# Performance work log

Hardware: AMD Instinct MI355X
Metric: run time of the kernel (lower is better)

## Reference

```python
import jax, jax.numpy as jnp
import numpy as np

V = 45      # vocab / input_size / output_size
H = 2048    # hidden_size
W = 128     # stack_width
D = 200     # stack_depth


def setup_inputs() -> dict:
    key = jax.random.key(0)
    ks = jax.random.split(key, 14)
    s = 0.02
    return {
        "inp": jax.random.randint(ks[0], (1,), 0, V),
        "hidden": jax.random.normal(ks[1], (1, 1, H), jnp.float32),
        "stack": jax.random.normal(ks[2], (1, D, W), jnp.float32),
        "emb": jax.random.normal(ks[3], (V, H), jnp.float32) * s,
        "ctrl_W": jax.random.normal(ks[4], (3, H), jnp.float32) * s,
        "ctrl_b": jnp.zeros((3,), jnp.float32),
        "sin_W": jax.random.normal(ks[5], (W, H), jnp.float32) * s,
        "sin_b": jnp.zeros((W,), jnp.float32),
        "w_ih": jax.random.normal(ks[6], (3 * H, H + W), jnp.float32) * s,
        "w_hh": jax.random.normal(ks[7], (3 * H, H), jnp.float32) * s,
        "b_ih": jnp.zeros((3 * H,), jnp.float32),
        "b_hh": jnp.zeros((3 * H,), jnp.float32),
        "dec_W": jax.random.normal(ks[8], (V, H), jnp.float32) * s,
        "dec_b": jnp.zeros((V,), jnp.float32),
    }


def reference(inp, hidden, stack, emb, ctrl_W, ctrl_b, sin_W, sin_b,
              w_ih, w_hh, b_ih, b_hh, dec_W, dec_b):
    h = hidden[0]  # [1, H]  (n_layers=1, unidirectional -> squeeze(0))

    # --- differentiable stack update ---
    controls = jax.nn.softmax(h @ ctrl_W.T + ctrl_b, axis=1)      # [1, 3]
    stack_input = jnp.tanh(h @ sin_W.T + sin_b)[:, None, :]       # [1, 1, W]
    zeros_bottom = jnp.zeros((1, 1, W), stack.dtype)
    stack_down = jnp.concatenate([stack[:, 1:], zeros_bottom], axis=1)   # pop
    stack_up = jnp.concatenate([stack_input, stack[:, :-1]], axis=1)    # push
    c = controls.reshape(1, 3, 1, 1)  # (push, pop, no_op)
    new_stack = c[:, 2] * stack + c[:, 0] * stack_up + c[:, 1] * stack_down
    stack_top = new_stack[:, 0, :]  # [1, W]

    # --- embed token, concat stack top ---
    x = jnp.concatenate([emb[inp].reshape(1, -1), stack_top], axis=1)  # [1, H+W]

    # --- GRU cell (PyTorch gate convention) ---
    gi = x @ w_ih.T + b_ih   # [1, 3H]
    gh = h @ w_hh.T + b_hh   # [1, 3H]
    i_r, i_z, i_n = jnp.split(gi, 3, axis=1)
    h_r, h_z, h_n = jnp.split(gh, 3, axis=1)
    r = jax.nn.sigmoid(i_r + h_r)
    z = jax.nn.sigmoid(i_z + h_z)
    n = jnp.tanh(i_n + r * h_n)
    h_new = (1.0 - z) * n + z * h   # [1, H]

    # --- decoder ---
    output = h_new @ dec_W.T + dec_b  # [1, V]
    return output, h_new[None], new_stack
```

## Files before the change

kernel.cpp:

```cpp
#include <hip/hip_runtime.h>

#define V_SZ 45
#define H_SZ 2048
#define W_SZ 128
#define D_SZ 200
#define X_SZ (H_SZ + W_SZ)
#define STACK_BLKS ((D_SZ * W_SZ) / 256)

#define WS_CTRL 0
#define WS_SIN  16
#define WS_HNEW 160

typedef float f4 __attribute__((ext_vector_type(4)));

__device__ __forceinline__ float dot4(f4 a, f4 b) {
  return a.x * b.x + a.y * b.y + a.z * b.z + a.w * b.w;
}

__device__ __forceinline__ f4 ldnt(const f4* p) {
  return __builtin_nontemporal_load(p);
}

__device__ __forceinline__ float wave_reduce(float v) {
#pragma unroll
  for (int o = 32; o > 0; o >>= 1) v += __shfl_down(v, o, 64);
  return v;
}

__device__ __forceinline__ void ctrl_softmax(const float* __restrict__ ws,
                                             float& c0, float& c1, float& c2) {
  const float l0 = ws[WS_CTRL + 0], l1 = ws[WS_CTRL + 1], l2 = ws[WS_CTRL + 2];
  const float m = fmaxf(l0, fmaxf(l1, l2));
  const float e0 = __expf(l0 - m), e1 = __expf(l1 - m), e2 = __expf(l2 - m);
  const float inv = 1.f / (e0 + e1 + e2);
  c0 = e0 * inv; c1 = e1 * inv; c2 = e2 * inv;
}

__global__ __launch_bounds__(256) void k1_small_gemv(
    const float* __restrict__ hidden,
    const float* __restrict__ ctrl_W,
    const float* __restrict__ ctrl_b,
    const float* __restrict__ sin_W,
    const float* __restrict__ sin_b,
    float* __restrict__ ws) {
  const int b = blockIdx.x;
  const int tid = threadIdx.x;
  const float* row = (b < 3) ? (ctrl_W + (size_t)b * H_SZ)
                             : (sin_W + (size_t)(b - 3) * H_SZ);
  const f4* rw4 = (const f4*)row;
  const f4* rh4 = (const f4*)hidden;
  float acc = dot4(rw4[tid], rh4[tid]) + dot4(rw4[tid + 256], rh4[tid + 256]);

  acc = wave_reduce(acc);
  __shared__ float red[4];
  const int wv_id = tid >> 6;
  if ((tid & 63) == 0) red[wv_id] = acc;
  __syncthreads();
  if (tid == 0) {
    float total = red[0] + red[1] + red[2] + red[3];
    if (b < 3) {
      ws[WS_CTRL + b] = total + ctrl_b[b];
    } else {
      ws[WS_SIN + (b - 3)] = tanhf(total + sin_b[b - 3]);
    }
  }
}

__global__ __launch_bounds__(256) void k3_gru_stack(
    const int* __restrict__ inp,
    const float* __restrict__ hidden,
    const float* __restrict__ emb,
    const float* __restrict__ stack,
    const float* __restrict__ w_ih,
    const float* __restrict__ w_hh,
    const float* __restrict__ b_ih,
    const float* __restrict__ b_hh,
    float* __restrict__ ws,
    float* __restrict__ out) {
  const int tid = threadIdx.x;

  if (blockIdx.x < STACK_BLKS) {
    const int i = blockIdx.x * 256 + tid;
    float c0, c1, c2;
    ctrl_softmax(ws, c0, c1, c2);
    const int d = i >> 7;
    const int w = i & (W_SZ - 1);
    const float s = stack[i];
    const float up = (d == 0) ? ws[WS_SIN + w] : stack[i - W_SZ];
    const float dn = (d == D_SZ - 1) ? 0.f : stack[i + W_SZ];
    out[V_SZ + H_SZ + i] = c2 * s + c0 * up + c1 * dn;
    return;
  }

  const int j = blockIdx.x - STACK_BLKS;

  float bi0 = 0.f, bi1 = 0.f, bi2 = 0.f;
  float bh0 = 0.f, bh1 = 0.f, bh2 = 0.f, hj = 0.f;
  if (tid == 0) {
    bi0 = b_ih[j]; bi1 = b_ih[j + H_SZ]; bi2 = b_ih[j + 2 * H_SZ];
    bh0 = b_hh[j]; bh1 = b_hh[j + H_SZ]; bh2 = b_hh[j + 2 * H_SZ];
    hj  = hidden[j];
  }

  float a0 = 0.f, a1 = 0.f, a2 = 0.f, a3 = 0.f, a4 = 0.f, a5 = 0.f;

  const f4* wi0 = (const f4*)(w_ih + (size_t)j * X_SZ);
  const f4* wi1 = (const f4*)(w_ih + (size_t)(j + H_SZ) * X_SZ);
  const f4* wi2 = (const f4*)(w_ih + (size_t)(j + 2 * H_SZ) * X_SZ);
  const f4* emb4 = (const f4*)(emb + (size_t)inp[0] * H_SZ);

#pragma unroll
  for (int q = 0; q < 2; ++q) {
    const int c = tid + q * 256;
    const f4 xv = emb4[c];
    a0 += dot4(ldnt(wi0 + c), xv);
    a1 += dot4(ldnt(wi1 + c), xv);
    a2 += dot4(ldnt(wi2 + c), xv);
  }
  if (tid < (X_SZ - H_SZ) / 4) {
    const int c = 512 + tid;
    const int w = 4 * tid;
    float c0, c1, c2;
    ctrl_softmax(ws, c0, c1, c2);
    const f4 s0 = *(const f4*)(stack + w);
    const f4 s1 = *(const f4*)(stack + W_SZ + w);
    const f4 sv = *(const f4*)(ws + WS_SIN + w);
    f4 xv;
    xv.x = c2 * s0.x + c0 * sv.x + c1 * s1.x;
    xv.y = c2 * s0.y + c0 * sv.y + c1 * s1.y;
    xv.z = c2 * s0.z + c0 * sv.z + c1 * s1.z;
    xv.w = c2 * s0.w + c0 * sv.w + c1 * s1.w;
    a0 += dot4(ldnt(wi0 + c), xv);
    a1 += dot4(ldnt(wi1 + c), xv);
    a2 += dot4(ldnt(wi2 + c), xv);
  }

  const f4* wh0 = (const f4*)(w_hh + (size_t)j * H_SZ);
  const f4* wh1 = (const f4*)(w_hh + (size_t)(j + H_SZ) * H_SZ);
  const f4* wh2 = (const f4*)(w_hh + (size_t)(j + 2 * H_SZ) * H_SZ);
  const f4* h4 = (const f4*)hidden;
#pragma unroll
  for (int q = 0; q < 2; ++q) {
    const int c = tid + q * 256;
    const f4 hv = h4[c];
    a3 += dot4(ldnt(wh0 + c), hv);
    a4 += dot4(ldnt(wh1 + c), hv);
    a5 += dot4(ldnt(wh2 + c), hv);
  }

  a0 = wave_reduce(a0); a1 = wave_reduce(a1); a2 = wave_reduce(a2);
  a3 = wave_reduce(a3); a4 = wave_reduce(a4); a5 = wave_reduce(a5);
  __shared__ float red[4][6];
  const int wv_id = tid >> 6;
  if ((tid & 63) == 0) {
    red[wv_id][0] = a0; red[wv_id][1] = a1; red[wv_id][2] = a2;
    red[wv_id][3] = a3; red[wv_id][4] = a4; red[wv_id][5] = a5;
  }
  __syncthreads();
  if (tid == 0) {
    float t[6];
#pragma unroll
    for (int q = 0; q < 6; ++q)
      t[q] = red[0][q] + red[1][q] + red[2][q] + red[3][q];
    const float gi_r = t[0] + bi0;
    const float gi_z = t[1] + bi1;
    const float gi_n = t[2] + bi2;
    const float gh_r = t[3] + bh0;
    const float gh_z = t[4] + bh1;
    const float gh_n = t[5] + bh2;
    const float r = 1.f / (1.f + __expf(-(gi_r + gh_r)));
    const float z = 1.f / (1.f + __expf(-(gi_z + gh_z)));
    const float n = tanhf(gi_n + r * gh_n);
    const float hn = (1.f - z) * n + z * hj;
    ws[WS_HNEW + j] = hn;
    out[V_SZ + j] = hn;
  }
}

__global__ __launch_bounds__(256) void k4_dec(
    const float* __restrict__ dec_W,
    const float* __restrict__ dec_b,
    const float* __restrict__ ws,
    float* __restrict__ out) {
  const int v = blockIdx.x;
  const int tid = threadIdx.x;
  float db = 0.f;
  if (tid == 0) db = dec_b[v];
  const f4* row = (const f4*)(dec_W + (size_t)v * H_SZ);
  const f4* h4 = (const f4*)(ws + WS_HNEW);
  float acc = dot4(row[tid], h4[tid]) + dot4(row[tid + 256], h4[tid + 256]);
  acc = wave_reduce(acc);
  __shared__ float red[4];
  const int wv_id = tid >> 6;
  if ((tid & 63) == 0) red[wv_id] = acc;
  __syncthreads();
  if (tid == 0) out[v] = red[0] + red[1] + red[2] + red[3] + db;
}

extern "C" void kernel_launch(void* const* d_in, const int* in_sizes, int n_in,
                              void* d_out, int out_size, void* d_ws, size_t ws_size,
                              hipStream_t stream) {
  const int*   inp    = (const int*)d_in[0];
  const float* hidden = (const float*)d_in[1];
  const float* stack  = (const float*)d_in[2];
  const float* emb    = (const float*)d_in[3];
  const float* ctrl_W = (const float*)d_in[4];
  const float* ctrl_b = (const float*)d_in[5];
  const float* sin_W  = (const float*)d_in[6];
  const float* sin_b  = (const float*)d_in[7];
  const float* w_ih   = (const float*)d_in[8];
  const float* w_hh   = (const float*)d_in[9];
  const float* b_ih   = (const float*)d_in[10];
  const float* b_hh   = (const float*)d_in[11];
  const float* dec_W  = (const float*)d_in[12];
  const float* dec_b  = (const float*)d_in[13];
  float* out = (float*)d_out;
  float* ws = (float*)d_ws;

  k1_small_gemv<<<3 + W_SZ, 256, 0, stream>>>(hidden, ctrl_W, ctrl_b, sin_W, sin_b, ws);
  k3_gru_stack<<<STACK_BLKS + H_SZ, 256, 0, stream>>>(inp, hidden, emb, stack,
                                                      w_ih, w_hh, b_ih, b_hh, ws, out);
  k4_dec<<<V_SZ, 256, 0, stream>>>(dec_W, dec_b, ws, out);
}
```

Before: 156.2 us.

## Overlap control GEMV with hidden/embedding GRU partial sums, finish stack part later

Moves the large GRU GEMV work that does not depend on the stack (embedding part of w_ih and all of w_hh) into the first kernel, which now runs alongside the control/stack-input GEMV. Partial gate sums go to workspace. A second kernel does the stack update, the 128-wide stack-top slice of w_ih (one wave per hidden unit) and the gate nonlinearities. This removes the serial dependency of the big weight stream on the small first kernel. In exchange it adds a workspace round trip for 6 partials per unit and a separate pass over the w_ih tail columns.

```diff
diff --git a/kernel.cpp b/kernel.cpp
--- a/kernel.cpp
+++ b/kernel.cpp
@@ -6,10 +6,13 @@
 #define D_SZ 200
 #define X_SZ (H_SZ + W_SZ)
 #define STACK_BLKS ((D_SZ * W_SZ) / 256)
+#define K1_BLKS (3 + W_SZ)
+#define GATE_JPB 4
+#define GATE_BLKS (H_SZ / GATE_JPB)
 
 #define WS_CTRL 0
 #define WS_SIN  16
-#define WS_HNEW 160
+#define WS_PART 160
 
 typedef float f4 __attribute__((ext_vector_type(4)));
 
@@ -24,6 +27,12 @@
 __device__ __forceinline__ float wave_reduce(float v) {
 #pragma unroll
   for (int o = 32; o > 0; o >>= 1) v += __shfl_down(v, o, 64);
+  return v;
+}
+
+__device__ __forceinline__ float half_reduce(float v) {
+#pragma unroll
+  for (int o = 16; o > 0; o >>= 1) v += __shfl_down(v, o, 32);
   return v;
 }
 
@@ -36,45 +45,101 @@
   c0 = e0 * inv; c1 = e1 * inv; c2 = e2 * inv;
 }
 
-__global__ __launch_bounds__(256) void k1_small_gemv(
+__global__ __launch_bounds__(256) void kA(
+    const int* __restrict__ inp,
     const float* __restrict__ hidden,
+    const float* __restrict__ emb,
     const float* __restrict__ ctrl_W,
     const float* __restrict__ ctrl_b,
     const float* __restrict__ sin_W,
     const float* __restrict__ sin_b,
-    float* __restrict__ ws) {
-  const int b = blockIdx.x;
-  const int tid = threadIdx.x;
-  const float* row = (b < 3) ? (ctrl_W + (size_t)b * H_SZ)
-                             : (sin_W + (size_t)(b - 3) * H_SZ);
-  const f4* rw4 = (const f4*)row;
-  const f4* rh4 = (const f4*)hidden;
-  float acc = dot4(rw4[tid], rh4[tid]) + dot4(rw4[tid + 256], rh4[tid + 256]);
-
-  acc = wave_reduce(acc);
-  __shared__ float red[4];
-  const int wv_id = tid >> 6;
-  if ((tid & 63) == 0) red[wv_id] = acc;
-  __syncthreads();
-  if (tid == 0) {
-    float total = red[0] + red[1] + red[2] + red[3];
-    if (b < 3) {
-      ws[WS_CTRL + b] = total + ctrl_b[b];
-    } else {
-      ws[WS_SIN + (b - 3)] = tanhf(total + sin_b[b - 3]);
-    }
-  }
-}
-
-__global__ __launch_bounds__(256) void k3_gru_stack(
-    const int* __restrict__ inp,
-    const float* __restrict__ hidden,
-    const float* __restrict__ emb,
-    const float* __restrict__ stack,
     const float* __restrict__ w_ih,
     const float* __restrict__ w_hh,
     const float* __restrict__ b_ih,
     const float* __restrict__ b_hh,
+    float* __restrict__ ws) {
+  const int tid = threadIdx.x;
+
+  if (blockIdx.x < K1_BLKS) {
+    const int b = blockIdx.x;
+    const float* row = (b < 3) ? (ctrl_W + (size_t)b * H_SZ)
+                               : (sin_W + (size_t)(b - 3) * H_SZ);
+    const f4* rw4 = (const f4*)row;
+    const f4* rh4 = (const f4*)hidden;
+    float acc = dot4(rw4[tid], rh4[tid]) + dot4(rw4[tid + 256], rh4[tid + 256]);
+    acc = wave_reduce(acc);
+    __shared__ float red1[4];
+    const int wv_id = tid >> 6;
+    if ((tid & 63) == 0) red1[wv_id] = acc;
+    __syncthreads();
+    if (tid == 0) {
+      float total = red1[0] + red1[1] + red1[2] + red1[3];
+      if (b < 3) ws[WS_CTRL + b] = total + ctrl_b[b];
+      else       ws[WS_SIN + (b - 3)] = tanhf(total + sin_b[b - 3]);
+    }
+    return;
+  }
+
+  const int j = blockIdx.x - K1_BLKS;
+
+  float bi0 = 0.f, bi1 = 0.f, bi2 = 0.f, bh0 = 0.f, bh1 = 0.f, bh2 = 0.f;
+  if (tid == 0) {
+    bi0 = b_ih[j]; bi1 = b_ih[j + H_SZ]; bi2 = b_ih[j + 2 * H_SZ];
+    bh0 = b_hh[j]; bh1 = b_hh[j + H_SZ]; bh2 = b_hh[j + 2 * H_SZ];
+  }
+
+  float a0 = 0.f, a1 = 0.f, a2 = 0.f, a3 = 0.f, a4 = 0.f, a5 = 0.f;
+
+  const f4* wi0 = (const f4*)(w_ih + (size_t)j * X_SZ);
+  const f4* wi1 = (const f4*)(w_ih + (size_t)(j + H_SZ) * X_SZ);
+  const f4* wi2 = (const f4*)(w_ih + (size_t)(j + 2 * H_SZ) * X_SZ);
+  const f4* emb4 = (const f4*)(emb + (size_t)inp[0] * H_SZ);
+#pragma unroll
+  for (int q = 0; q < 2; ++q) {
+    const int c = tid + q * 256;
+    const f4 xv = emb4[c];
+    a0 += dot4(ldnt(wi0 + c), xv);
+    a1 += dot4(ldnt(wi1 + c), xv);
+    a2 += dot4(ldnt(wi2 + c), xv);
+  }
+
+  const f4* wh0 = (const f4*)(w_hh + (size_t)j * H_SZ);
+  const f4* wh1 = (const f4*)(w_hh + (size_t)(j + H_SZ) * H_SZ);
+  const f4* wh2 = (const f4*)(w_hh + (size_t)(j + 2 * H_SZ) * H_SZ);
+  const f4* h4 = (const f4*)hidden;
+#pragma unroll
+  for (int q = 0; q < 2; ++q) {
+    const int c = tid + q * 256;
+    const f4 hv = h4[c];
+    a3 += dot4(ldnt(wh0 + c), hv);
+    a4 += dot4(ldnt(wh1 + c), hv);
+    a5 += dot4(ldnt(wh2 + c), hv);
+  }
+
+  a0 = wave_reduce(a0); a1 = wave_reduce(a1); a2 = wave_reduce(a2);
+  a3 = wave_reduce(a3); a4 = wave_reduce(a4); a5 = wave_reduce(a5);
+  __shared__ float red[4][6];
+  const int wv_id = tid >> 6;
+  if ((tid & 63) == 0) {
+    red[wv_id][0] = a0; red[wv_id][1] = a1; red[wv_id][2] = a2;
+    red[wv_id][3] = a3; red[wv_id][4] = a4; red[wv_id][5] = a5;
+  }
+  __syncthreads();
+  if (tid == 0) {
+    float* p = ws + WS_PART + 6 * j;
+    p[0] = red[0][0] + red[1][0] + red[2][0] + red[3][0] + bi0;
+    p[1] = red[0][1] + red[1][1] + red[2][1] + red[3][1] + bi1;
+    p[2] = red[0][2] + red[1][2] + red[2][2] + red[3][2] + bi2;
+    p[3] = red[0][3] + red[1][3] + red[2][3] + red[3][3] + bh0;
+    p[4] = red[0][4] + red[1][4] + red[2][4] + red[3][4] + bh1;
+    p[5] = red[0][5] + red[1][5] + red[2][5] + red[3][5] + bh2;
+  }
+}
+
+__global__ __launch_bounds__(256) void kB(
+    const float* __restrict__ hidden,
+    const float* __restrict__ stack,
+    const float* __restrict__ w_ih,
     float* __restrict__ ws,
     float* __restrict__ out) {
   const int tid = threadIdx.x;
@@ -92,102 +157,62 @@
     return;
   }
 
-  const int j = blockIdx.x - STACK_BLKS;
-
-  float bi0 = 0.f, bi1 = 0.f, bi2 = 0.f;
-  float bh0 = 0.f, bh1 = 0.f, bh2 = 0.f, hj = 0.f;
-  if (tid == 0) {
-    bi0 = b_ih[j]; bi1 = b_ih[j + H_SZ]; bi2 = b_ih[j + 2 * H_SZ];
-    bh0 = b_hh[j]; bh1 = b_hh[j + H_SZ]; bh2 = b_hh[j + 2 * H_SZ];
-    hj  = hidden[j];
-  }
-
-  float a0 = 0.f, a1 = 0.f, a2 = 0.f, a3 = 0.f, a4 = 0.f, a5 = 0.f;
-
-  const f4* wi0 = (const f4*)(w_ih + (size_t)j * X_SZ);
-  const f4* wi1 = (const f4*)(w_ih + (size_t)(j + H_SZ) * X_SZ);
-  const f4* wi2 = (const f4*)(w_ih + (size_t)(j + 2 * H_SZ) * X_SZ);
-  const f4* emb4 = (const f4*)(emb + (size_t)inp[0] * H_SZ);
-
-#pragma unroll
-  for (int q = 0; q < 2; ++q) {
-    const int c = tid + q * 256;
-    const f4 xv = emb4[c];
-    a0 += dot4(ldnt(wi0 + c), xv);
-    a1 += dot4(ldnt(wi1 + c), xv);
-    a2 += dot4(ldnt(wi2 + c), xv);
-  }
-  if (tid < (X_SZ - H_SZ) / 4) {
-    const int c = 512 + tid;
-    const int w = 4 * tid;
-    float c0, c1, c2;
-    ctrl_softmax(ws, c0, c1, c2);
-    const f4 s0 = *(const f4*)(stack + w);
-    const f4 s1 = *(const f4*)(stack + W_SZ + w);
-    const f4 sv = *(const f4*)(ws + WS_SIN + w);
-    f4 xv;
-    xv.x = c2 * s0.x + c0 * sv.x + c1 * s1.x;
-    xv.y = c2 * s0.y + c0 * sv.y + c1 * s1.y;
-    xv.z = c2 * s0.z + c0 * sv.z + c1 * s1.z;
-    xv.w = c2 * s0.w + c0 * sv.w + c1 * s1.w;
-    a0 += dot4(ldnt(wi0 + c), xv);
-    a1 += dot4(ldnt(wi1 + c), xv);
-    a2 += dot4(ldnt(wi2 + c), xv);
-  }
-
-  const f4* wh0 = (const f4*)(w_hh + (size_t)j * H_SZ);
-  const f4* wh1 = (const f4*)(w_hh + (size_t)(j + H_SZ) * H_SZ);
-  const f4* wh2 = (const f4*)(w_hh + (size_t)(j + 2 * H_SZ) * H_SZ);
-  const f4* h4 = (const f4*)hidden;
-#pragma unroll
-  for (int q = 0; q < 2; ++q) {
-    const int c = tid + q * 256;
-    const f4 hv = h4[c];
-    a3 += dot4(ldnt(wh0 + c), hv);
-    a4 += dot4(ldnt(wh1 + c), hv);
-    a5 += dot4(ldnt(wh2 + c), hv);
-  }
-
-  a0 = wave_reduce(a0); a1 = wave_reduce(a1); a2 = wave_reduce(a2);
-  a3 = wave_reduce(a3); a4 = wave_reduce(a4); a5 = wave_reduce(a5);
-  __shared__ float red[4][6];
-  const int wv_id = tid >> 6;
-  if ((tid & 63) == 0) {
-    red[wv_id][0] = a0; red[wv_id][1] = a1; red[wv_id][2] = a2;
-    red[wv_id][3] = a3; red[wv_id][4] = a4; red[wv_id][5] = a5;
-  }
-  __syncthreads();
-  if (tid == 0) {
-    float t[6];
-#pragma unroll
-    for (int q = 0; q < 6; ++q)
-      t[q] = red[0][q] + red[1][q] + red[2][q] + red[3][q];
-    const float gi_r = t[0] + bi0;
-    const float gi_z = t[1] + bi1;
-    const float gi_n = t[2] + bi2;
-    const float gh_r = t[3] + bh0;
-    const float gh_z = t[4] + bh1;
-    const float gh_n = t[5] + bh2;
+  const int wv = tid >> 6;
+  const int lane = tid & 63;
+  const int j = (blockIdx.x - STACK_BLKS) * GATE_JPB + wv;
+  const int half = lane >> 5;
+  const int c = lane & 31;
+
+  float hj = 0.f;
+  if (lane == 0) hj = hidden[j];
+
+  float c0, c1, c2;
+  ctrl_softmax(ws, c0, c1, c2);
+  const f4 s0 = *(const f4*)(stack + 4 * c);
+  const f4 s1 = *(const f4*)(stack + W_SZ + 4 * c);
+  const f4 sv = *(const f4*)(ws + WS_SIN + 4 * c);
+  f4 xv;
+  xv.x = c2 * s0.x + c0 * sv.x + c1 * s1.x;
+  xv.y = c2 * s0.y + c0 * sv.y + c1 * s1.y;
+  xv.z = c2 * s0.z + c0 * sv.z + c1 * s1.z;
+  xv.w = c2 * s0.w + c0 * sv.w + c1 * s1.w;
+
+  const f4* t0 = (const f4*)(w_ih + (size_t)j * X_SZ + H_SZ);
+  const f4* t1 = (const f4*)(w_ih + (size_t)(j + H_SZ) * X_SZ + H_SZ);
+  const f4* t2 = (const f4*)(w_ih + (size_t)(j + 2 * H_SZ) * X_SZ + H_SZ);
+
+  float v01 = dot4(ldnt((half ? t1 : t0) + c), xv);
+  float v2 = half ? 0.f : dot4(ldnt(t2 + c), xv);
+
+  v01 = half_reduce(v01);
+  v2 = half_reduce(v2);
+  const float d1 = __shfl(v01, 32, 64);
+
+  if (lane == 0) {
+    const float* p = ws + WS_PART + 6 * j;
+    const float gi_r = p[0] + v01;
+    const float gi_z = p[1] + d1;
+    const float gi_n = p[2] + v2;
+    const float gh_r = p[3];
+    const float gh_z = p[4];
+    const float gh_n = p[5];
     const float r = 1.f / (1.f + __expf(-(gi_r + gh_r)));
     const float z = 1.f / (1.f + __expf(-(gi_z + gh_z)));
     const float n = tanhf(gi_n + r * gh_n);
-    const float hn = (1.f - z) * n + z * hj;
-    ws[WS_HNEW + j] = hn;
-    out[V_SZ + j] = hn;
-  }
-}
-
-__global__ __launch_bounds__(256) void k4_dec(
+    out[V_SZ + j] = (1.f - z) * n + z * hj;
+  }
+}
+
+__global__ __launch_bounds__(256) void kC(
     const float* __restrict__ dec_W,
     const float* __restrict__ dec_b,
-    const float* __restrict__ ws,
     float* __restrict__ out) {
   const int v = blockIdx.x;
   const int tid = threadIdx.x;
   float db = 0.f;
   if (tid == 0) db = dec_b[v];
   const f4* row = (const f4*)(dec_W + (size_t)v * H_SZ);
-  const f4* h4 = (const f4*)(ws + WS_HNEW);
+  const f4* h4 = (const f4*)(out + V_SZ);
   float acc = dot4(row[tid], h4[tid]) + dot4(row[tid + 256], h4[tid + 256]);
   acc = wave_reduce(acc);
   __shared__ float red[4];
@@ -217,8 +242,8 @@
   float* out = (float*)d_out;
   float* ws = (float*)d_ws;
 
-  k1_small_gemv<<<3 + W_SZ, 256, 0, stream>>>(hidden, ctrl_W, ctrl_b, sin_W, sin_b, ws);
-  k3_gru_stack<<<STACK_BLKS + H_SZ, 256, 0, stream>>>(inp, hidden, emb, stack,
-                                                      w_ih, w_hh, b_ih, b_hh, ws, out);
-  k4_dec<<<V_SZ, 256, 0, stream>>>(dec_W, dec_b, ws, out);
-}
+  kA<<<K1_BLKS + H_SZ, 256, 0, stream>>>(inp, hidden, emb, ctrl_W, ctrl_b,
+                                         sin_W, sin_b, w_ih, w_hh, b_ih, b_hh, ws);
+  kB<<<STACK_BLKS + GATE_BLKS, 256, 0, stream>>>(hidden, stack, w_ih, ws, out);
+  kC<<<V_SZ, 256, 0, stream>>>(dec_W, dec_b, out);
+}
```

Result: no change. 154.1 us (-1.3%).
